# Kernel optimization log

Hardware: AMD Instinct MI355X
Metric: run time of the kernel (lower is better)

## Reference

```python
import jax, jax.numpy as jnp
import numpy as np

B, N, E = 2, 10000, 80000
NODE_DIM, EDGE_DIM = 30, 3
H, VE, EE = 64, 16, 16  # encoder_hidden_dim -> width AND depth of hidden chain


def _mlp_params(key, din, h, dout, prefix):
    k = jax.random.split(key, 6)
    s_in, s_h = 1.0 / np.sqrt(din), 1.0 / np.sqrt(h)
    return {
        prefix + '_Win': jax.random.normal(k[0], (din, h), jnp.float32) * s_in,
        prefix + '_bin': jax.random.normal(k[1], (h,), jnp.float32) * s_in,
        prefix + '_Whid': jax.random.normal(k[2], (h, h, h), jnp.float32) * s_h,  # h stacked hidden Linears
        prefix + '_bhid': jax.random.normal(k[3], (h, h), jnp.float32) * s_h,
        prefix + '_Wout': jax.random.normal(k[4], (h, dout), jnp.float32) * s_h,
        prefix + '_bout': jax.random.normal(k[5], (dout,), jnp.float32) * s_h,
    }


def setup_inputs() -> dict:
    key = jax.random.key(0)
    ks = jax.random.split(key, 8)
    inp = {
        'nodes': jax.random.normal(ks[0], (B, N, NODE_DIM), jnp.float32),
        'globals_': jax.random.normal(ks[1], (B,), jnp.float32),
        'edges': jax.random.normal(ks[2], (B, E, EDGE_DIM), jnp.float32),
        'senders': jax.random.randint(ks[3], (B, E), 0, N, jnp.int32),
        'receivers': jax.random.randint(ks[4], (B, E), 0, N, jnp.int32),
    }
    inp.update(_mlp_params(ks[5], NODE_DIM + 1, H, VE, 'node'))  # +1 global col
    inp.update(_mlp_params(ks[6], EDGE_DIM + 4, H, EE, 'edge'))  # +4 relative feats
    return inp


def _chain(x, Win, b_in, Whid, bhid, Wout, bout):
    # Linear(in,h) -> h x Linear(h,h) -> Linear(h,out); NO nonlinearity (matches source)
    h = x @ Win + b_in
    def step(c, wb):
        W, b = wb
        return c @ W + b, None
    h, _ = jax.lax.scan(step, h, (Whid, bhid))
    return h @ Wout + bout


def reference(nodes, globals_, edges, senders, receivers,
              node_Win, node_bin, node_Whid, node_bhid, node_Wout, node_bout,
              edge_Win, edge_bin, edge_Whid, edge_bhid, edge_Wout, edge_bout):
    Bv, Nv = nodes.shape[0], nodes.shape[1]
    g = jnp.broadcast_to(globals_[:, None, None], (Bv, Nv, 1))
    nodes_g = jnp.concatenate([nodes, g], axis=-1)  # [B,N,node_dim+1]
    pos = nodes_g[..., :3]  # first 3 features are 3D positions
    gather = jax.vmap(lambda p, idx: p[idx])
    s = gather(pos, senders)    # [B,E,3]
    r = gather(pos, receivers)  # [B,E,3]
    d = s - r
    norm = jnp.linalg.norm(d, axis=-1, keepdims=True)
    edges_full = jnp.concatenate([edges, d, norm], axis=-1)  # [B,E,edge_dim+4]
    latent_nodes = _chain(nodes_g, node_Win, node_bin, node_Whid, node_bhid, node_Wout, node_bout)
    latent_edges = _chain(edges_full, edge_Win, edge_bin, edge_Whid, edge_bhid, edge_Wout, edge_bout)
    return latent_nodes, latent_edges
```

## Files before the change

kernel.cpp:

```cpp
#include <hip/hip_runtime.h>

#define NN 10000
#define EE_ 80000
#define NODE_ROWS 20000
#define NODE_BLOCKS 79
#define EDGE_BLOCKS 625

typedef float f4 __attribute__((ext_vector_type(4)));

#define GLD4(g, l) __builtin_amdgcn_global_load_lds(                      \
    (const __attribute__((address_space(1))) void*)(g),                   \
    (__attribute__((address_space(3))) void*)(l), 16, 0, 0)
#define GLD1(g, l) __builtin_amdgcn_global_load_lds(                      \
    (const __attribute__((address_space(1))) void*)(g),                   \
    (__attribute__((address_space(3))) void*)(l), 4, 0, 0)

__global__ __launch_bounds__(256) void chunk_kernel(
    const float* __restrict__ nWhid, const float* __restrict__ nbhid,
    const float* __restrict__ eWhid, const float* __restrict__ ebhid,
    float* __restrict__ pt)
{
  const int t = threadIdx.x;
  const int c = blockIdx.x >> 4;
  const int j = blockIdx.x & 15;
  const float* Wh = c ? eWhid : nWhid;
  const float* bh = c ? ebhid : nbhid;
  const int L0 = 4*j;

  __shared__ float s_at[2][64*68];
  __shared__ float s_b[65*64];
  __shared__ float s_bp[256];

  for (int idx = t; idx < 4160; idx += 256) {
    int r = idx >> 6, k = idx & 63;
    s_at[0][k*68 + r] = (r < 64) ? Wh[(size_t)L0*4096 + idx] : bh[L0*64 + k];
  }
  int cur = 0;
  #pragma unroll 1
  for (int s = 1; s <= 3; ++s) {
    const float* WB = Wh + (size_t)(L0 + s)*4096;
    const float* bB = bh + (size_t)(L0 + s)*64;
    #pragma unroll
    for (int i = 0; i < 4; ++i) {
      int i4 = t + i*256;
      *(float4*)&s_b[i4*4] = *(const float4*)&WB[i4*4];
    }
    if (t < 16) *(float4*)&s_b[4096 + t*4] = *(const float4*)&bB[t*4];
    __syncthreads();

    const int ti = t >> 4, tj = t & 15;
    float acc[4][4];
    #pragma unroll
    for (int d = 0; d < 4; ++d)
      #pragma unroll
      for (int e = 0; e < 4; ++e) acc[d][e] = 0.f;
    #pragma unroll 4
    for (int k = 0; k < 64; ++k) {
      float4 a4 = *(const float4*)&s_at[cur][k*68 + 4*ti];
      float4 b4 = *(const float4*)&s_b[k*64 + 4*tj];
      float av[4] = {a4.x, a4.y, a4.z, a4.w};
      float bv[4] = {b4.x, b4.y, b4.z, b4.w};
      #pragma unroll
      for (int d = 0; d < 4; ++d)
        #pragma unroll
        for (int e = 0; e < 4; ++e) acc[d][e] += av[d]*bv[e];
    }
    {
      int cc = t & 63, kq = t >> 6;
      float p = 0.f;
      #pragma unroll 4
      for (int kk = 0; kk < 16; ++kk) {
        int k = kq*16 + kk;
        p += s_at[cur][k*68 + 64] * s_b[k*64 + cc];
      }
      s_bp[kq*64 + cc] = p;
    }
    __syncthreads();
    if (s < 3) {
      #pragma unroll
      for (int d = 0; d < 4; ++d)
        #pragma unroll
        for (int e = 0; e < 4; ++e)
          s_at[cur^1][(4*tj + e)*68 + 4*ti + d] = acc[d][e];
      if (t < 64)
        s_at[cur^1][t*68 + 64] =
            s_bp[t] + s_bp[64+t] + s_bp[128+t] + s_bp[192+t] + s_b[4096+t];
      __syncthreads();
      cur ^= 1;
    } else {
      float* D = pt + (size_t)(c*16 + j)*4160;
      #pragma unroll
      for (int d = 0; d < 4; ++d)
        *(float4*)&D[(4*ti + d)*64 + 4*tj] =
            make_float4(acc[d][0], acc[d][1], acc[d][2], acc[d][3]);
      if (t < 64)
        D[4096 + t] = s_bp[t] + s_bp[64+t] + s_bp[128+t] + s_bp[192+t] + s_b[4096+t];
    }
  }
}

__global__ __launch_bounds__(256, 1) void fold16_kernel(
    const float* __restrict__ nWin, const float* __restrict__ nbin,
    const float* __restrict__ nWout, const float* __restrict__ nbout,
    const float* __restrict__ eWin, const float* __restrict__ ebin,
    const float* __restrict__ eWout, const float* __restrict__ ebout,
    const float* __restrict__ pt, float* __restrict__ ws)
{
  const int tid  = threadIdx.x;
  const int lane = tid & 63;
  const int wv   = __builtin_amdgcn_readfirstlane(tid >> 6);
  const int c = blockIdx.x >> 4;
  const int q = blockIdx.x & 15;
  const float* Win  = c ? eWin  : nWin;
  const float* bin  = c ? ebin  : nbin;
  const float* Wout = c ? eWout : nWout;
  const float* bout = c ? ebout : nbout;
  const float* PT = pt + (size_t)c*16*4160;
  const int din = c ? 7 : 31;
  float* weff = ws + (c ? 512 : 0);

  __shared__ float lds_f[13312];

  const int r4 = lane >> 4, c16 = lane & 15;
  const int oE = r4*64 + ((c16 ^ r4) << 2);
  const int oO = r4*64 + ((c16 ^ (4 | r4)) << 2);
  const int swz = lane & 7;
  const int aw0 = lane*256 + (((4*wv + 0) ^ swz) << 4);
  const int aw1 = lane*256 + (((4*wv + 1) ^ swz) << 4);
  const int aw2 = lane*256 + (((4*wv + 2) ^ swz) << 4);
  const int aw3 = lane*256 + (((4*wv + 3) ^ swz) << 4);
  const int ab  = 16384 + wv*256 + lane*4;
  const int apw = 52224 + lane*16 + wv*4;
  const int apr = 52224 + lane*16;

  float vlane = Wout[lane*16 + q];
  float bpart = 0.f;
  const int kbase = 16*wv;
  float s[16];
  #pragma unroll
  for (int j = 0; j < 16; ++j)
    s[j] = __uint_as_float(__builtin_amdgcn_readlane(__float_as_uint(vlane), kbase + j));

#define STAGE(BF, L) do {                                                 \
    const float* gW_ = PT + (size_t)(L)*4160 + wv*1024;                   \
    float* lW_ = lds_f + (BF)*4352 + wv*1024;                             \
    GLD4(gW_ +   0 + oE, lW_ +   0);                                      \
    GLD4(gW_ + 256 + oO, lW_ + 256);                                      \
    GLD4(gW_ + 512 + oE, lW_ + 512);                                      \
    GLD4(gW_ + 768 + oO, lW_ + 768);                                      \
    GLD1(PT + (size_t)(L)*4160 + 4096 + lane,                             \
         lds_f + (BF)*4352 + 4096 + wv*64);                               \
  } while (0)

#define CSTEP(OFS, VMC, STAGESTMT) do {                                   \
    STAGESTMT;                                                            \
    asm volatile("s_waitcnt vmcnt(" #VMC ") lgkmcnt(0)" ::: "memory");    \
    __builtin_amdgcn_s_barrier();           \
    f4 f0_, f1_, f2_, f3_; float bb_;                                     \
    asm volatile("ds_read_b128 %0, %5 offset:" #OFS "\n\t"                \
                 "ds_read_b128 %1, %6 offset:" #OFS "\n\t"                \
                 "ds_read_b128 %2, %7 offset:" #OFS "\n\t"                \
                 "ds_read_b128 %3, %8 offset:" #OFS "\n\t"                \
                 "ds_read_b32  %4, %9 offset:" #OFS "\n\t"                \
                 "s_waitcnt lgkmcnt(0)"                                   \
                 : "=&v"(f0_), "=&v"(f1_), "=&v"(f2_), "=&v"(f3_), "=&v"(bb_) \
                 : "v"(aw0), "v"(aw1), "v"(aw2), "v"(aw3), "v"(ab)        \
                 : "memory");                                             \
    __builtin_amdgcn_sched_barrier(0);                                    \
    bpart = __builtin_fmaf(bb_, vlane, bpart);                            \
    float a0_ = __builtin_fmaf(f0_.y, s[1],  f0_.x * s[0]);               \
    a0_ = __builtin_fmaf(f0_.z, s[2],  a0_);                              \
    a0_ = __builtin_fmaf(f0_.w, s[3],  a0_);                              \
    float a1_ = __builtin_fmaf(f1_.y, s[5],  f1_.x * s[4]);               \
    a1_ = __builtin_fmaf(f1_.z, s[6],  a1_);                              \
    a1_ = __builtin_fmaf(f1_.w, s[7],  a1_);                              \
    float a2_ = __builtin_fmaf(f2_.y, s[9],  f2_.x * s[8]);               \
    a2_ = __builtin_fmaf(f2_.z, s[10], a2_);                              \
    a2_ = __builtin_fmaf(f2_.w, s[11], a2_);                              \
    float a3_ = __builtin_fmaf(f3_.y, s[13], f3_.x * s[12]);              \
    a3_ = __builtin_fmaf(f3_.z, s[14], a3_);                              \
    a3_ = __builtin_fmaf(f3_.w, s[15], a3_);                              \
    float acc_ = (a0_ + a1_) + (a2_ + a3_);                               \
    asm volatile("ds_write_b32 %0, %1\n\t"                                \
                 "s_waitcnt lgkmcnt(0)"                                   \
                 :: "v"(apw), "v"(acc_) : "memory");                      \
    __builtin_amdgcn_s_barrier();                   \
    f4 p4_;                                                               \
    asm volatile("ds_read_b128 %0, %1\n\t"                                \
                 "s_waitcnt lgkmcnt(0)"                                   \
                 : "=&v"(p4_) : "v"(apr) : "memory");                     \
    __builtin_amdgcn_sched_barrier(0);                                    \
    vlane = (p4_.x + p4_.y) + (p4_.z + p4_.w);                            \
    _Pragma("unroll")                                                     \
    for (int jj = 0; jj < 16; ++jj)                                       \
      s[jj] = __uint_as_float(__builtin_amdgcn_readlane(                  \
                  __float_as_uint(vlane), kbase + jj));                   \
  } while (0)

  STAGE(0, 15);
  STAGE(1, 14);

  int L = 15;
  #pragma unroll 1
  for (int ii = 0; ii < 4; ++ii) {
    CSTEP(0,     10, STAGE(2, L-2));
    CSTEP(17408, 10, STAGE(0, L-3));
    CSTEP(34816, 10, STAGE(1, L-4));
    L -= 3;
  }
  CSTEP(0,     10, STAGE(2, 1));
  CSTEP(17408, 10, STAGE(0, 0));
  CSTEP(34816, 5,  (void)0);
  CSTEP(0,     0,  (void)0);
#undef CSTEP
#undef STAGE

  if (wv != 0) return;

  float red = __builtin_fmaf(bin[lane], vlane, bpart);
  #pragma unroll
  for (int off = 32; off > 0; off >>= 1) red += __shfl_xor(red, off, 64);

  float* sv = lds_f;
  sv[lane] = vlane;
  __builtin_amdgcn_sched_barrier(0);

  if (lane == din) {
    weff[din*16 + q] = red + bout[q];
  } else if (lane < din) {
    float a0 = 0.f, a1 = 0.f, a2 = 0.f, a3 = 0.f;
    const float* wr = Win + (size_t)lane*64;
    #pragma unroll
    for (int kb = 0; kb < 16; ++kb) {
      f4 vv = *(const f4*)&sv[kb*4];
      f4 wv4 = *(const f4*)&wr[kb*4];
      a0 = __builtin_fmaf(wv4.x, vv.x, a0);
      a1 = __builtin_fmaf(wv4.y, vv.y, a1);
      a2 = __builtin_fmaf(wv4.z, vv.z, a2);
      a3 = __builtin_fmaf(wv4.w, vv.w, a3);
    }
    weff[lane*16 + q] = (a0 + a1) + (a2 + a3);
  }
}

template<int NF>
static __device__ __forceinline__ void mlp_apply_store(const float* x, const float* sW,
                                                       float* po)
{
  float a[16];
  #pragma unroll
  for (int q = 0; q < 16; ++q) a[q] = sW[NF*16 + q];
  #pragma unroll
  for (int j = 0; j < NF; ++j) {
    const float xv = x[j];
    #pragma unroll
    for (int q = 0; q < 16; ++q) a[q] += xv * sW[j*16 + q];
  }
  float4* d = (float4*)po;
  d[0] = make_float4(a[0],  a[1],  a[2],  a[3]);
  d[1] = make_float4(a[4],  a[5],  a[6],  a[7]);
  d[2] = make_float4(a[8],  a[9],  a[10], a[11]);
  d[3] = make_float4(a[12], a[13], a[14], a[15]);
}

__global__ __launch_bounds__(256) void apply_kernel(
    const float* __restrict__ nodes, const float* __restrict__ globals_,
    const float* __restrict__ edges, const int* __restrict__ senders,
    const int* __restrict__ receivers, const float* __restrict__ ws,
    float* __restrict__ out)
{
  __shared__ float sW[32*16];
  const bool is_node = (blockIdx.x < NODE_BLOCKS);
  {
    const float* src = is_node ? ws : ws + 512;
    const int n = is_node ? 32*16 : 8*16;
    for (int j = threadIdx.x; j < n; j += 256) sW[j] = src[j];
  }
  __syncthreads();

  if (is_node) {
    const int rn = blockIdx.x*256 + threadIdx.x;
    if (rn >= NODE_ROWS) return;
    float x[31];
    const float* p = nodes + (size_t)rn*30;
    #pragma unroll
    for (int j = 0; j < 15; ++j) {
      float2 u = *(const float2*)(p + j*2);
      x[2*j]     = u.x;
      x[2*j + 1] = u.y;
    }
    const int b = (rn >= NN) ? 1 : 0;
    x[30] = globals_[b];
    mlp_apply_store<31>(x, sW, out + (size_t)rn*16);
  } else {
    const int re = (blockIdx.x - NODE_BLOCKS)*256 + threadIdx.x;
    const int b = (re >= EE_) ? 1 : 0;
    float x[7];
    const float* ep = edges + (size_t)re*3;
    x[0] = ep[0]; x[1] = ep[1]; x[2] = ep[2];
    const int si = senders[re], ri = receivers[re];
    const float* ps = nodes + ((size_t)(b*NN + si))*30;
    const float* pr = nodes + ((size_t)(b*NN + ri))*30;
    const float dx = ps[0] - pr[0];
    const float dy = ps[1] - pr[1];
    const float dz = ps[2] - pr[2];
    x[3] = dx; x[4] = dy; x[5] = dz;
    x[6] = sqrtf(dx*dx + dy*dy + dz*dz);
    mlp_apply_store<7>(x, sW, out + (size_t)(NODE_ROWS + re)*16);
  }
}

extern "C" void kernel_launch(void* const* d_in, const int* in_sizes, int n_in,
                              void* d_out, int out_size, void* d_ws, size_t ws_size,
                              hipStream_t stream)
{
  const float* nodes    = (const float*)d_in[0];
  const float* globals_ = (const float*)d_in[1];
  const float* edges    = (const float*)d_in[2];
  const int* senders   = (const int*)d_in[3];
  const int* receivers = (const int*)d_in[4];
  const float* nWin  = (const float*)d_in[5];
  const float* nbin  = (const float*)d_in[6];
  const float* nWhid = (const float*)d_in[7];
  const float* nbhid = (const float*)d_in[8];
  const float* nWout = (const float*)d_in[9];
  const float* nbout = (const float*)d_in[10];
  const float* eWin  = (const float*)d_in[11];
  const float* ebin  = (const float*)d_in[12];
  const float* eWhid = (const float*)d_in[13];
  const float* ebhid = (const float*)d_in[14];
  const float* eWout = (const float*)d_in[15];
  const float* ebout = (const float*)d_in[16];
  float* ws  = (float*)d_ws;
  float* out = (float*)d_out;
  float* pt  = ws + 1024;

  chunk_kernel<<<32, 256, 0, stream>>>(nWhid, nbhid, eWhid, ebhid, pt);

  fold16_kernel<<<32, 256, 0, stream>>>(
      nWin, nbin, nWout, nbout, eWin, ebin, eWout, ebout, pt, ws);

  apply_kernel<<<NODE_BLOCKS + EDGE_BLOCKS, 256, 0, stream>>>(
      nodes, globals_, edges, senders, receivers, ws, out);
}
```

Baseline: 36.91 us.

## Merge chunk and fold kernels into one cooperative kernel with grid sync

Combines the two weight-collapse kernels (chunk products of hidden layers and the 16-step fold) into a single cooperative launch. A grid-wide barrier replaces the kernel boundary, and shared memory is carved from one buffer reused by both phases. The aim is to drop one kernel launch and its inter-kernel gap. In exchange it pays for a cooperative launch and a grid sync, which on AMD can cost as much as a launch boundary.

```diff
diff --git a/kernel.cpp b/kernel.cpp
--- a/kernel.cpp
+++ b/kernel.cpp
@@ -1,4 +1,7 @@
 #include <hip/hip_runtime.h>
+#include <hip/hip_cooperative_groups.h>
+
+namespace cg = cooperative_groups;
 
 #define NN 10000
 #define EE_ 80000
@@ -15,131 +18,132 @@
     (const __attribute__((address_space(1))) void*)(g),                   \
     (__attribute__((address_space(3))) void*)(l), 4, 0, 0)
 
-__global__ __launch_bounds__(256) void chunk_kernel(
+__global__ __launch_bounds__(256, 1) void collapse_kernel(
+    const float* __restrict__ nWin, const float* __restrict__ nbin,
     const float* __restrict__ nWhid, const float* __restrict__ nbhid,
+    const float* __restrict__ nWout, const float* __restrict__ nbout,
+    const float* __restrict__ eWin, const float* __restrict__ ebin,
     const float* __restrict__ eWhid, const float* __restrict__ ebhid,
-    float* __restrict__ pt)
+    const float* __restrict__ eWout, const float* __restrict__ ebout,
+    float* __restrict__ ws)
 {
+  __shared__ float smem[13312];
   const int t = threadIdx.x;
-  const int c = blockIdx.x >> 4;
-  const int j = blockIdx.x & 15;
-  const float* Wh = c ? eWhid : nWhid;
-  const float* bh = c ? ebhid : nbhid;
-  const int L0 = 4*j;
-
-  __shared__ float s_at[2][64*68];
-  __shared__ float s_b[65*64];
-  __shared__ float s_bp[256];
-
-  for (int idx = t; idx < 4160; idx += 256) {
-    int r = idx >> 6, k = idx & 63;
-    s_at[0][k*68 + r] = (r < 64) ? Wh[(size_t)L0*4096 + idx] : bh[L0*64 + k];
-  }
-  int cur = 0;
-  #pragma unroll 1
-  for (int s = 1; s <= 3; ++s) {
-    const float* WB = Wh + (size_t)(L0 + s)*4096;
-    const float* bB = bh + (size_t)(L0 + s)*64;
-    #pragma unroll
-    for (int i = 0; i < 4; ++i) {
-      int i4 = t + i*256;
-      *(float4*)&s_b[i4*4] = *(const float4*)&WB[i4*4];
-    }
-    if (t < 16) *(float4*)&s_b[4096 + t*4] = *(const float4*)&bB[t*4];
-    __syncthreads();
-
-    const int ti = t >> 4, tj = t & 15;
-    float acc[4][4];
-    #pragma unroll
-    for (int d = 0; d < 4; ++d)
+  const int c  = blockIdx.x >> 4;
+  const int jq = blockIdx.x & 15;
+  float* pt = ws + 1024;
+
+  {
+    float* s_at = smem;
+    float* s_b  = smem + 8704;
+    float* s_bp = smem + 12864;
+    const float* Wh = c ? eWhid : nWhid;
+    const float* bh = c ? ebhid : nbhid;
+    const int L0 = 4*jq;
+
+    for (int idx = t; idx < 4160; idx += 256) {
+      int r = idx >> 6, k = idx & 63;
+      s_at[k*68 + r] = (r < 64) ? Wh[(size_t)L0*4096 + idx] : bh[L0*64 + k];
+    }
+    int cur = 0;
+    #pragma unroll 1
+    for (int s = 1; s <= 3; ++s) {
+      const float* WB = Wh + (size_t)(L0 + s)*4096;
+      const float* bB = bh + (size_t)(L0 + s)*64;
       #pragma unroll
-      for (int e = 0; e < 4; ++e) acc[d][e] = 0.f;
-    #pragma unroll 4
-    for (int k = 0; k < 64; ++k) {
-      float4 a4 = *(const float4*)&s_at[cur][k*68 + 4*ti];
-      float4 b4 = *(const float4*)&s_b[k*64 + 4*tj];
-      float av[4] = {a4.x, a4.y, a4.z, a4.w};
-      float bv[4] = {b4.x, b4.y, b4.z, b4.w};
+      for (int i = 0; i < 4; ++i) {
+        int i4 = t + i*256;
+        *(float4*)&s_b[i4*4] = *(const float4*)&WB[i4*4];
+      }
+      if (t < 16) *(float4*)&s_b[4096 + t*4] = *(const float4*)&bB[t*4];
+      __syncthreads();
+
+      const int ti = t >> 4, tj = t & 15;
+      float acc[4][4];
       #pragma unroll
       for (int d = 0; d < 4; ++d)
         #pragma unroll
-        for (int e = 0; e < 4; ++e) acc[d][e] += av[d]*bv[e];
-    }
-    {
-      int cc = t & 63, kq = t >> 6;
-      float p = 0.f;
+        for (int e = 0; e < 4; ++e) acc[d][e] = 0.f;
       #pragma unroll 4
-      for (int kk = 0; kk < 16; ++kk) {
-        int k = kq*16 + kk;
-        p += s_at[cur][k*68 + 64] * s_b[k*64 + cc];
-      }
-      s_bp[kq*64 + cc] = p;
-    }
-    __syncthreads();
-    if (s < 3) {
-      #pragma unroll
-      for (int d = 0; d < 4; ++d)
+      for (int k = 0; k < 64; ++k) {
+        float4 a4 = *(const float4*)&s_at[cur*4352 + k*68 + 4*ti];
+        float4 b4 = *(const float4*)&s_b[k*64 + 4*tj];
+        float av[4] = {a4.x, a4.y, a4.z, a4.w};
+        float bv[4] = {b4.x, b4.y, b4.z, b4.w};
         #pragma unroll
-        for (int e = 0; e < 4; ++e)
-          s_at[cur^1][(4*tj + e)*68 + 4*ti + d] = acc[d][e];
-      if (t < 64)
-        s_at[cur^1][t*68 + 64] =
-            s_bp[t] + s_bp[64+t] + s_bp[128+t] + s_bp[192+t] + s_b[4096+t];
+        for (int d = 0; d < 4; ++d)
+          #pragma unroll
+          for (int e = 0; e < 4; ++e) acc[d][e] += av[d]*bv[e];
+      }
+      {
+        int cc = t & 63, kq = t >> 6;
+        float p = 0.f;
+        #pragma unroll 4
+        for (int kk = 0; kk < 16; ++kk) {
+          int k = kq*16 + kk;
+          p += s_at[cur*4352 + k*68 + 64] * s_b[k*64 + cc];
+        }
+        s_bp[kq*64 + cc] = p;
+      }
       __syncthreads();
-      cur ^= 1;
-    } else {
-      float* D = pt + (size_t)(c*16 + j)*4160;
-      #pragma unroll
-      for (int d = 0; d < 4; ++d)
-        *(float4*)&D[(4*ti + d)*64 + 4*tj] =
-            make_float4(acc[d][0], acc[d][1], acc[d][2], acc[d][3]);
-      if (t < 64)
-        D[4096 + t] = s_bp[t] + s_bp[64+t] + s_bp[128+t] + s_bp[192+t] + s_b[4096+t];
-    }
-  }
-}
-
-__global__ __launch_bounds__(256, 1) void fold16_kernel(
-    const float* __restrict__ nWin, const float* __restrict__ nbin,
-    const float* __restrict__ nWout, const float* __restrict__ nbout,
-    const float* __restrict__ eWin, const float* __restrict__ ebin,
-    const float* __restrict__ eWout, const float* __restrict__ ebout,
-    const float* __restrict__ pt, float* __restrict__ ws)
-{
-  const int tid  = threadIdx.x;
-  const int lane = tid & 63;
-  const int wv   = __builtin_amdgcn_readfirstlane(tid >> 6);
-  const int c = blockIdx.x >> 4;
-  const int q = blockIdx.x & 15;
-  const float* Win  = c ? eWin  : nWin;
-  const float* bin  = c ? ebin  : nbin;
-  const float* Wout = c ? eWout : nWout;
-  const float* bout = c ? ebout : nbout;
-  const float* PT = pt + (size_t)c*16*4160;
-  const int din = c ? 7 : 31;
-  float* weff = ws + (c ? 512 : 0);
-
-  __shared__ float lds_f[13312];
-
-  const int r4 = lane >> 4, c16 = lane & 15;
-  const int oE = r4*64 + ((c16 ^ r4) << 2);
-  const int oO = r4*64 + ((c16 ^ (4 | r4)) << 2);
-  const int swz = lane & 7;
-  const int aw0 = lane*256 + (((4*wv + 0) ^ swz) << 4);
-  const int aw1 = lane*256 + (((4*wv + 1) ^ swz) << 4);
-  const int aw2 = lane*256 + (((4*wv + 2) ^ swz) << 4);
-  const int aw3 = lane*256 + (((4*wv + 3) ^ swz) << 4);
-  const int ab  = 16384 + wv*256 + lane*4;
-  const int apw = 52224 + lane*16 + wv*4;
-  const int apr = 52224 + lane*16;
-
-  float vlane = Wout[lane*16 + q];
-  float bpart = 0.f;
-  const int kbase = 16*wv;
-  float s[16];
-  #pragma unroll
-  for (int j = 0; j < 16; ++j)
-    s[j] = __uint_as_float(__builtin_amdgcn_readlane(__float_as_uint(vlane), kbase + j));
+      if (s < 3) {
+        #pragma unroll
+        for (int d = 0; d < 4; ++d)
+          #pragma unroll
+          for (int e = 0; e < 4; ++e)
+            s_at[(cur^1)*4352 + (4*tj + e)*68 + 4*ti + d] = acc[d][e];
+        if (t < 64)
+          s_at[(cur^1)*4352 + t*68 + 64] =
+              s_bp[t] + s_bp[64+t] + s_bp[128+t] + s_bp[192+t] + s_b[4096+t];
+        __syncthreads();
+        cur ^= 1;
+      } else {
+        float* D = pt + (size_t)(c*16 + jq)*4160;
+        #pragma unroll
+        for (int d = 0; d < 4; ++d)
+          *(float4*)&D[(4*ti + d)*64 + 4*tj] =
+              make_float4(acc[d][0], acc[d][1], acc[d][2], acc[d][3]);
+        if (t < 64)
+          D[4096 + t] = s_bp[t] + s_bp[64+t] + s_bp[128+t] + s_bp[192+t] + s_b[4096+t];
+      }
+    }
+  }
+
+  __threadfence();
+  cg::this_grid().sync();
+
+  {
+    float* lds_f = smem;
+    const int lane = t & 63;
+    const int wv   = __builtin_amdgcn_readfirstlane(t >> 6);
+    const int q = jq;
+    const float* Win  = c ? eWin  : nWin;
+    const float* bin  = c ? ebin  : nbin;
+    const float* Wout = c ? eWout : nWout;
+    const float* bout = c ? ebout : nbout;
+    const float* PT = pt + (size_t)c*16*4160;
+    const int din = c ? 7 : 31;
+    float* weff = ws + (c ? 512 : 0);
+
+    const int r4 = lane >> 4, c16 = lane & 15;
+    const int oE = r4*64 + ((c16 ^ r4) << 2);
+    const int oO = r4*64 + ((c16 ^ (4 | r4)) << 2);
+    const int swz = lane & 7;
+    const int aw0 = lane*256 + (((4*wv + 0) ^ swz) << 4);
+    const int aw1 = lane*256 + (((4*wv + 1) ^ swz) << 4);
+    const int aw2 = lane*256 + (((4*wv + 2) ^ swz) << 4);
+    const int aw3 = lane*256 + (((4*wv + 3) ^ swz) << 4);
+    const int ab  = 16384 + wv*256 + lane*4;
+    const int apw = 52224 + lane*16 + wv*4;
+    const int apr = 52224 + lane*16;
+
+    float vlane = Wout[lane*16 + q];
+    float bpart = 0.f;
+    const int kbase = 16*wv;
+    float s[16];
+    #pragma unroll
+    for (int j = 0; j < 16; ++j)
+      s[j] = __uint_as_float(__builtin_amdgcn_readlane(__float_as_uint(vlane), kbase + j));
 
 #define STAGE(BF, L) do {                                                 \
     const float* gW_ = PT + (size_t)(L)*4160 + wv*1024;                   \
@@ -155,7 +159,7 @@
 #define CSTEP(OFS, VMC, STAGESTMT) do {                                   \
     STAGESTMT;                                                            \
     asm volatile("s_waitcnt vmcnt(" #VMC ") lgkmcnt(0)" ::: "memory");    \
-    __builtin_amdgcn_s_barrier();           \
+    __builtin_amdgcn_s_barrier();                                         \
     f4 f0_, f1_, f2_, f3_; float bb_;                                     \
     asm volatile("ds_read_b128 %0, %5 offset:" #OFS "\n\t"                \
                  "ds_read_b128 %1, %6 offset:" #OFS "\n\t"                \
@@ -184,7 +188,7 @@
     asm volatile("ds_write_b32 %0, %1\n\t"                                \
                  "s_waitcnt lgkmcnt(0)"                                   \
                  :: "v"(apw), "v"(acc_) : "memory");                      \
-    __builtin_amdgcn_s_barrier();                   \
+    __builtin_amdgcn_s_barrier();                                         \
     f4 p4_;                                                               \
     asm volatile("ds_read_b128 %0, %1\n\t"                                \
                  "s_waitcnt lgkmcnt(0)"                                   \
@@ -197,49 +201,50 @@
                   __float_as_uint(vlane), kbase + jj));                   \
   } while (0)
 
-  STAGE(0, 15);
-  STAGE(1, 14);
-
-  int L = 15;
-  #pragma unroll 1
-  for (int ii = 0; ii < 4; ++ii) {
-    CSTEP(0,     10, STAGE(2, L-2));
-    CSTEP(17408, 10, STAGE(0, L-3));
-    CSTEP(34816, 10, STAGE(1, L-4));
-    L -= 3;
-  }
-  CSTEP(0,     10, STAGE(2, 1));
-  CSTEP(17408, 10, STAGE(0, 0));
-  CSTEP(34816, 5,  (void)0);
-  CSTEP(0,     0,  (void)0);
+    STAGE(0, 15);
+    STAGE(1, 14);
+
+    int L = 15;
+    #pragma unroll 1
+    for (int ii = 0; ii < 4; ++ii) {
+      CSTEP(0,     10, STAGE(2, L-2));
+      CSTEP(17408, 10, STAGE(0, L-3));
+      CSTEP(34816, 10, STAGE(1, L-4));
+      L -= 3;
+    }
+    CSTEP(0,     10, STAGE(2, 1));
+    CSTEP(17408, 10, STAGE(0, 0));
+    CSTEP(34816, 5,  (void)0);
+    CSTEP(0,     0,  (void)0);
 #undef CSTEP
 #undef STAGE
 
-  if (wv != 0) return;
-
-  float red = __builtin_fmaf(bin[lane], vlane, bpart);
-  #pragma unroll
-  for (int off = 32; off > 0; off >>= 1) red += __shfl_xor(red, off, 64);
-
-  float* sv = lds_f;
-  sv[lane] = vlane;
-  __builtin_amdgcn_sched_barrier(0);
-
-  if (lane == din) {
-    weff[din*16 + q] = red + bout[q];
-  } else if (lane < din) {
-    float a0 = 0.f, a1 = 0.f, a2 = 0.f, a3 = 0.f;
-    const float* wr = Win + (size_t)lane*64;
+    if (wv != 0) return;
+
+    float red = __builtin_fmaf(bin[lane], vlane, bpart);
     #pragma unroll
-    for (int kb = 0; kb < 16; ++kb) {
-      f4 vv = *(const f4*)&sv[kb*4];
-      f4 wv4 = *(const f4*)&wr[kb*4];
-      a0 = __builtin_fmaf(wv4.x, vv.x, a0);
-      a1 = __builtin_fmaf(wv4.y, vv.y, a1);
-      a2 = __builtin_fmaf(wv4.z, vv.z, a2);
-      a3 = __builtin_fmaf(wv4.w, vv.w, a3);
-    }
-    weff[lane*16 + q] = (a0 + a1) + (a2 + a3);
+    for (int off = 32; off > 0; off >>= 1) red += __shfl_xor(red, off, 64);
+
+    float* sv = lds_f;
+    sv[lane] = vlane;
+    __builtin_amdgcn_sched_barrier(0);
+
+    if (lane == din) {
+      weff[din*16 + q] = red + bout[q];
+    } else if (lane < din) {
+      float a0 = 0.f, a1 = 0.f, a2 = 0.f, a3 = 0.f;
+      const float* wr = Win + (size_t)lane*64;
+      #pragma unroll
+      for (int kb = 0; kb < 16; ++kb) {
+        f4 vv = *(const f4*)&sv[kb*4];
+        f4 wv4 = *(const f4*)&wr[kb*4];
+        a0 = __builtin_fmaf(wv4.x, vv.x, a0);
+        a1 = __builtin_fmaf(wv4.y, vv.y, a1);
+        a2 = __builtin_fmaf(wv4.z, vv.z, a2);
+        a3 = __builtin_fmaf(wv4.w, vv.w, a3);
+      }
+      weff[lane*16 + q] = (a0 + a1) + (a2 + a3);
+    }
   }
 }
 
@@ -333,12 +338,15 @@
   const float* ebout = (const float*)d_in[16];
   float* ws  = (float*)d_ws;
   float* out = (float*)d_out;
-  float* pt  = ws + 1024;
-
-  chunk_kernel<<<32, 256, 0, stream>>>(nWhid, nbhid, eWhid, ebhid, pt);
-
-  fold16_kernel<<<32, 256, 0, stream>>>(
-      nWin, nbin, nWout, nbout, eWin, ebin, eWout, ebout, pt, ws);
+
+  void* args[] = {
+    (void*)&nWin, (void*)&nbin, (void*)&nWhid, (void*)&nbhid,
+    (void*)&nWout, (void*)&nbout,
+    (void*)&eWin, (void*)&ebin, (void*)&eWhid, (void*)&ebhid,
+    (void*)&eWout, (void*)&ebout, (void*)&ws
+  };
+  hipLaunchCooperativeKernel((void*)collapse_kernel, dim3(32), dim3(256),
+                             args, 0, stream);
 
   apply_kernel<<<NODE_BLOCKS + EDGE_BLOCKS, 256, 0, stream>>>(
       nodes, globals_, edges, senders, receivers, ws, out);
```

Measured after the change: 64.66 us. 75.2% more time.
